# Kernel tuning notes

Measured on AMD Instinct MI355X. Metric: run time of the kernel, lower is better.

The kernel has to match this reference:

```python
import math
import jax, jax.numpy as jnp
import numpy as np

N = 50000          # nodes
E = 1_600_000      # edges
DNE = 128
DED = 128
NUM_RBF = 50
R_CUT = 5.0
LN_EPS = 1e-5


def setup_inputs() -> dict:
    key = jax.random.key(0)
    ks = jax.random.split(key, 16)
    z = jax.random.normal(ks[0], (N, 25), jnp.float32)
    edge = jax.random.randint(ks[1], (E, 2), 0, N, dtype=jnp.int64)
    r = jax.random.uniform(ks[2], (E,), jnp.float32) * (R_CUT * 1.1)  # some beyond cutoff
    u_raw = jax.random.normal(ks[3], (E, 3), jnp.float32)
    u = u_raw / jnp.linalg.norm(u_raw, axis=-1, keepdims=True)

    def xavier(k, shape):
        fan_in, fan_out = shape
        lim = math.sqrt(6.0 / (fan_in + fan_out))
        return jax.random.uniform(k, shape, jnp.float32, -lim, lim)

    return {
        "z": z, "edge": edge, "r": r, "u": u,
        "A_na_w": xavier(ks[4], (25, DNE)), "A_na_b": jnp.zeros((DNE,), jnp.float32),
        "A_nbr_w": xavier(ks[5], (25, DNE)), "A_nbr_b": jnp.zeros((DNE,), jnp.float32),
        "W_ndp_w": xavier(ks[6], (NUM_RBF, DNE)), "W_ndp_b": jnp.zeros((DNE,), jnp.float32),
        "W_nrd_w": xavier(ks[7], (2 * DNE, DNE)), "W_nrd_b": jnp.zeros((DNE,), jnp.float32),
        "W_nru_w": xavier(ks[8], (DNE, DNE)), "W_nru_b": jnp.zeros((DNE,), jnp.float32),
        "W_erp_w": xavier(ks[9], (NUM_RBF, DED)), "W_erp_b": jnp.zeros((DED,), jnp.float32),
        "ln_g": jnp.ones((DNE,), jnp.float32), "ln_b": jnp.zeros((DNE,), jnp.float32),
    }


def _sh_l2(u):
    x, y, zc = u[:, 0], u[:, 1], u[:, 2]
    s3 = math.sqrt(3.0)
    return jnp.stack([
        s3 * x * y,
        s3 * y * zc,
        0.5 * (3.0 * zc * zc - 1.0),
        s3 * zc * x,
        0.5 * s3 * (x * x - y * y),
    ], axis=-1)  # [E, 5]


def _rbf(r):
    start = math.exp(-R_CUT)
    means = jnp.linspace(start, 1.0, NUM_RBF)
    beta = (2.0 / NUM_RBF * (1.0 - start)) ** (-2)
    alpha = 5.0 / R_CUT
    return jnp.exp(-beta * (jnp.exp(-alpha * r[:, None]) - means) ** 2)  # [E, NUM_RBF]


def reference(z, edge, r, u,
              A_na_w, A_na_b, A_nbr_w, A_nbr_b,
              W_ndp_w, W_ndp_b, W_nrd_w, W_nrd_b,
              W_nru_w, W_nru_b, W_erp_w, W_erp_b,
              ln_g, ln_b):
    i, j = edge[:, 0], edge[:, 1]
    n_nodes = z.shape[0]

    # edge tensor representations (Lmax=2)
    rt0 = r[:, None]          # [E,1]
    rt1 = u                   # [E,3]
    rt2 = _sh_l2(u)           # [E,5]

    rbf = _rbf(r)                                              # [E,R]
    c = (0.5 * (jnp.cos(math.pi * r / R_CUT) + 1.0)
         * (r < R_CUT).astype(r.dtype))[:, None]               # [E,1]

    nbr = jax.nn.silu(z @ A_nbr_w + A_nbr_b)                   # [N,dne]
    gate = (rbf @ W_ndp_w + W_ndp_b) * c                       # [E,dne]
    msg = nbr[j] * gate                                        # gather + gate
    m = jax.ops.segment_sum(msg, i, num_segments=n_nodes)      # scatter-add [N,dne]

    na = jax.nn.silu(z @ A_na_w + A_na_b)
    h = jnp.concatenate([na, m], axis=-1) @ W_nrd_w + W_nrd_b  # [N,dne]
    mu = jnp.mean(h, axis=-1, keepdims=True)
    var = jnp.var(h, axis=-1, keepdims=True)
    h = (h - mu) / jnp.sqrt(var + LN_EPS) * ln_g + ln_b
    h = jax.nn.silu(h)
    h = h @ W_nru_w + W_nru_b                                  # [N,dne]

    t = (h[i] + h[j]) * (rbf @ W_erp_w + W_erp_b)              # [E,ded]
    return (h, t, rt0, rt1, rt2, c)
```

## Files before the change

### kernel.cpp

```cpp
#include <hip/hip_runtime.h>
#include <hip/hip_bf16.h>
#include <math.h>

#define NN 50000
#define NE 1600000
#define D 128
#define NRBF 50
#define RCUT 5.0f
#define LNEPS 1e-5f
#define SCAN_B 196
#define NB 16
#define NPW 8
#define EO_GRID 2048

typedef __attribute__((ext_vector_type(8))) short bf16x8;
typedef __attribute__((ext_vector_type(4))) float f32x4;

__device__ __forceinline__ float silu_f(float x) {
    return x / (1.0f + __expf(-x));
}
__device__ __forceinline__ unsigned short f2bf(float x) {
    __hip_bfloat16 b = __float2bfloat16(x);
    return *reinterpret_cast<unsigned short*>(&b);
}
__device__ __forceinline__ float bf2f(unsigned short u) {
    unsigned int x = ((unsigned int)u) << 16;
    return __uint_as_float(x);
}

__global__ __launch_bounds__(128) void nbr_kernel(
    const float* __restrict__ z, const float* __restrict__ Aw,
    const float* __restrict__ Ab, unsigned short* __restrict__ nbr_bf)
{
    const int n = blockIdx.x;
    const int d = threadIdx.x;
    float acc = Ab[d];
#pragma unroll
    for (int k = 0; k < 25; ++k)
        acc = fmaf(z[n * 25 + k], Aw[k * D + d], acc);
    nbr_bf[(size_t)n * D + d] = f2bf(silu_f(acc));
}

__global__ __launch_bounds__(256) void aux_kernel(
    const int* __restrict__ edge, const float* __restrict__ r,
    const float* __restrict__ u, float* __restrict__ rt0,
    float* __restrict__ rt1, float* __restrict__ rt2,
    float* __restrict__ cout, int* __restrict__ cnt)
{
    const int e = blockIdx.x * 256 + threadIdx.x;
    if (e >= NE) return;
    const float rr = r[e];
    __builtin_nontemporal_store(rr, &rt0[e]);
    const float cc = (rr < RCUT)
        ? 0.5f * (__cosf(3.14159265358979f * rr * (1.0f / RCUT)) + 1.0f)
        : 0.0f;
    __builtin_nontemporal_store(cc, &cout[e]);
    const float x  = u[e * 3 + 0];
    const float y  = u[e * 3 + 1];
    const float zc = u[e * 3 + 2];
    __builtin_nontemporal_store(x,  &rt1[(size_t)e * 3 + 0]);
    __builtin_nontemporal_store(y,  &rt1[(size_t)e * 3 + 1]);
    __builtin_nontemporal_store(zc, &rt1[(size_t)e * 3 + 2]);
    const float s3 = 1.7320508075688772f;
    __builtin_nontemporal_store(s3 * x * y,                  &rt2[(size_t)e * 5 + 0]);
    __builtin_nontemporal_store(s3 * y * zc,                 &rt2[(size_t)e * 5 + 1]);
    __builtin_nontemporal_store(0.5f * (3.0f * zc * zc - 1.0f), &rt2[(size_t)e * 5 + 2]);
    __builtin_nontemporal_store(s3 * zc * x,                 &rt2[(size_t)e * 5 + 3]);
    __builtin_nontemporal_store(0.5f * s3 * (x * x - y * y), &rt2[(size_t)e * 5 + 4]);
    atomicAdd(&cnt[edge[2 * e]], 1);
}

__global__ __launch_bounds__(256) void scan1_kernel(
    const int* __restrict__ cnt, int* __restrict__ off, int* __restrict__ bsum)
{
    __shared__ int s[2][256];
    const int t = threadIdx.x;
    const int g = blockIdx.x * 256 + t;
    const int v = (g < NN) ? cnt[g] : 0;
    int incl = v;
    s[0][t] = incl;
    __syncthreads();
    int cur = 0;
#pragma unroll
    for (int dd = 1; dd < 256; dd <<= 1) {
        const int add = (t >= dd) ? s[cur][t - dd] : 0;
        incl += add;
        s[cur ^ 1][t] = incl;
        __syncthreads();
        cur ^= 1;
    }
    if (g < NN) off[g] = incl - v;
    if (t == 255) bsum[blockIdx.x] = incl;
}

__global__ __launch_bounds__(256) void scan2_kernel(int* __restrict__ bsum)
{
    __shared__ int s[2][256];
    const int t = threadIdx.x;
    const int v = (t < SCAN_B) ? bsum[t] : 0;
    int incl = v;
    s[0][t] = incl;
    __syncthreads();
    int cur = 0;
#pragma unroll
    for (int dd = 1; dd < 256; dd <<= 1) {
        const int add = (t >= dd) ? s[cur][t - dd] : 0;
        incl += add;
        s[cur ^ 1][t] = incl;
        __syncthreads();
        cur ^= 1;
    }
    if (t < SCAN_B) bsum[t] = incl - v;
}

__global__ __launch_bounds__(256) void scan3_kernel(
    int* __restrict__ off, const int* __restrict__ bsum)
{
    const int g = blockIdx.x * 256 + threadIdx.x;
    if (g < NN) off[g] += bsum[blockIdx.x];
    if (g == 0) off[NN] = NE;
}

__global__ __launch_bounds__(256) void scatter_kernel(
    const int* __restrict__ edge, const float* __restrict__ r,
    const int* __restrict__ off, int* __restrict__ cursor,
    uint2* __restrict__ jr)
{
    const int e = blockIdx.x * 256 + threadIdx.x;
    if (e >= NE) return;
    const int2 ep = ((const int2*)edge)[e];
    const int pos = atomicAdd(&cursor[ep.x], 1);
    uint2 v;
    v.x = (unsigned int)ep.y;
    v.y = __float_as_uint(r[e]);
    jr[off[ep.x] + pos] = v;
}

__global__ __launch_bounds__(256, 3) void gather_msg_wave(
    const uint2* __restrict__ jr, const int* __restrict__ off,
    const float* __restrict__ W_ndp, const float* __restrict__ b_ndp,
    const unsigned short* __restrict__ nbr_bf, float* __restrict__ m)
{
    const int tid = threadIdx.x;
    const int w   = tid >> 6;
    const int l   = tid & 63;
    const int lr  = l & 15;
    const int lg  = l >> 4;

    bf16x8 wf[8][2];
#pragma unroll
    for (int dt = 0; dt < 8; ++dt) {
        const int col = lr * 8 + dt;
#pragma unroll
        for (int s = 0; s < 2; ++s) {
            bf16x8 v;
#pragma unroll
            for (int j = 0; j < 8; ++j) {
                const int k = s * 32 + lg * 8 + j;
                float wv = 0.0f;
                if (k < NRBF)       wv = W_ndp[k * D + col];
                else if (k == NRBF) wv = b_ndp[col];
                v[j] = (short)f2bf(wv);
            }
            wf[dt][s] = v;
        }
    }

    const float start = expf(-RCUT);
    const float step  = (1.0f - start) / (NRBF - 1);
    const float bq    = (2.0f / NRBF) * (1.0f - start);
    const float beta  = 1.0f / (bq * bq);

    const int wid = blockIdx.x * 4 + w;

    for (int nn = 0; nn < NPW; ++nn) {
        const int n = wid * NPW + nn;
        if (n >= NN) break;
        const int s0  = off[n];
        const int deg = off[n + 1] - s0;

        f32x4 macc[8] = {{0,0,0,0},{0,0,0,0},{0,0,0,0},{0,0,0,0},
                         {0,0,0,0},{0,0,0,0},{0,0,0,0},{0,0,0,0}};

        uint2 v = make_uint2(0u, 0u);
        if (l < 16 && l < deg) v = jr[s0 + l];

        for (int base = 0; base < deg; base += 16) {
            const bool val = (l < 16) && (base + l < deg);
            const unsigned int jv = val ? v.x : 0u;
            float er = 0.0f, cc = 0.0f;
            if (val) {
                const float rr = __uint_as_float(v.y);
                er = __expf(-rr);
                cc = (rr < RCUT)
                    ? 0.5f * (__cosf(3.14159265358979f * rr * (1.0f / RCUT)) + 1.0f)
                    : 0.0f;
            }
            uint2 vn = make_uint2(0u, 0u);
            if (l < 16 && base + 16 + l < deg) vn = jr[s0 + base + 16 + l];

            const float erL = __shfl(er, lr);
            const float ccL = __shfl(cc, lr);

            bf16x8 nv0, nv1, nv2, nv3;
            {
                const int j0 = __shfl((int)jv, lg * 4 + 0);
                const int j1 = __shfl((int)jv, lg * 4 + 1);
                const int j2 = __shfl((int)jv, lg * 4 + 2);
                const int j3 = __shfl((int)jv, lg * 4 + 3);
                nv0 = *(const bf16x8*)(nbr_bf + (size_t)j0 * D + lr * 8);
                nv1 = *(const bf16x8*)(nbr_bf + (size_t)j1 * D + lr * 8);
                nv2 = *(const bf16x8*)(nbr_bf + (size_t)j2 * D + lr * 8);
                nv3 = *(const bf16x8*)(nbr_bf + (size_t)j3 * D + lr * 8);
            }

            bf16x8 af[2];
#pragma unroll
            for (int s = 0; s < 2; ++s) {
                bf16x8 a;
#pragma unroll
                for (int j = 0; j < 8; ++j) {
                    const int k = s * 32 + lg * 8 + j;
                    float pv = 0.0f;
                    if (k < NRBF) {
                        const float diff = erL - (start + (float)k * step);
                        pv = ccL * __expf(-beta * diff * diff);
                    } else if (k == NRBF) {
                        pv = ccL;
                    }
                    a[j] = (short)f2bf(pv);
                }
                af[s] = a;
            }

#pragma unroll
            for (int dt = 0; dt < 8; ++dt) {
                f32x4 acc = {0.0f, 0.0f, 0.0f, 0.0f};
                acc = __builtin_amdgcn_mfma_f32_16x16x32_bf16(af[0], wf[dt][0], acc, 0, 0, 0);
                acc = __builtin_amdgcn_mfma_f32_16x16x32_bf16(af[1], wf[dt][1], acc, 0, 0, 0);
                macc[dt][0] = fmaf(bf2f((unsigned short)nv0[dt]), acc[0], macc[dt][0]);
                macc[dt][1] = fmaf(bf2f((unsigned short)nv1[dt]), acc[1], macc[dt][1]);
                macc[dt][2] = fmaf(bf2f((unsigned short)nv2[dt]), acc[2], macc[dt][2]);
                macc[dt][3] = fmaf(bf2f((unsigned short)nv3[dt]), acc[3], macc[dt][3]);
            }
            v = vn;
        }

        float vv[8];
#pragma unroll
        for (int dt = 0; dt < 8; ++dt) {
            float x = macc[dt][0] + macc[dt][1] + macc[dt][2] + macc[dt][3];
            x += __shfl_xor(x, 16);
            x += __shfl_xor(x, 32);
            vv[dt] = x;
        }
        if (lg == 0) {
            f32x4 o0 = {vv[0], vv[1], vv[2], vv[3]};
            f32x4 o1 = {vv[4], vv[5], vv[6], vv[7]};
            float* mp = &m[(size_t)n * D + lr * 8];
            *(f32x4*)mp       = o0;
            *(f32x4*)(mp + 4) = o1;
        }
    }
}

__global__ __launch_bounds__(256) void node_kernel2(
    const float* __restrict__ z, const float* __restrict__ A_na_w,
    const float* __restrict__ A_na_b, const float* __restrict__ m,
    const float* __restrict__ W_nrd_w, const float* __restrict__ W_nrd_b,
    const float* __restrict__ W_nru_w, const float* __restrict__ W_nru_b,
    const float* __restrict__ ln_g, const float* __restrict__ ln_b,
    float* __restrict__ hout, unsigned short* __restrict__ h_bf)
{
    __shared__ float inbuf[NB][260];
    __shared__ float wbuf[32][128];
    __shared__ float part[4][NB][2];

    const int tid = threadIdx.x;
    const int n0 = blockIdx.x * NB;
    const int nl = tid & 15;
    const int dg = tid >> 4;

    for (int idx = tid; idx < NB * 128; idx += 256) {
        const int n = idx >> 7;
        const int d = idx & 127;
        float acc = A_na_b[d];
#pragma unroll
        for (int k = 0; k < 25; ++k)
            acc = fmaf(z[(size_t)(n0 + n) * 25 + k], A_na_w[k * D + d], acc);
        inbuf[n][d]       = silu_f(acc);
        inbuf[n][128 + d] = m[(size_t)(n0 + n) * D + d];
    }

    float h1[8];
#pragma unroll
    for (int dd = 0; dd < 8; ++dd) h1[dd] = W_nrd_b[dg * 8 + dd];

    for (int tile = 0; tile < 8; ++tile) {
        __syncthreads();
        for (int v = tid; v < 32 * 32; v += 256) {
            const int row = v >> 5;
            const int c4  = (v & 31) * 4;
            *(float4*)&wbuf[row][c4] =
                *(const float4*)&W_nrd_w[(size_t)(tile * 32 + row) * D + c4];
        }
        __syncthreads();
#pragma unroll 4
        for (int k = 0; k < 32; ++k) {
            const float rin = inbuf[nl][tile * 32 + k];
            const float4 wa = *(const float4*)&wbuf[k][dg * 8];
            const float4 wb = *(const float4*)&wbuf[k][dg * 8 + 4];
            h1[0] = fmaf(rin, wa.x, h1[0]);
            h1[1] = fmaf(rin, wa.y, h1[1]);
            h1[2] = fmaf(rin, wa.z, h1[2]);
            h1[3] = fmaf(rin, wa.w, h1[3]);
            h1[4] = fmaf(rin, wb.x, h1[4]);
            h1[5] = fmaf(rin, wb.y, h1[5]);
            h1[6] = fmaf(rin, wb.z, h1[6]);
            h1[7] = fmaf(rin, wb.w, h1[7]);
        }
    }

    float s = 0.0f, sq = 0.0f;
#pragma unroll
    for (int dd = 0; dd < 8; ++dd) { s += h1[dd]; sq += h1[dd] * h1[dd]; }
    s  += __shfl_xor(s, 16);  sq += __shfl_xor(sq, 16);
    s  += __shfl_xor(s, 32);  sq += __shfl_xor(sq, 32);
    const int wv = tid >> 6;
    if ((tid & 63) < 16) { part[wv][nl][0] = s; part[wv][nl][1] = sq; }
    __syncthreads();
    float ts = 0.0f, tsq = 0.0f;
#pragma unroll
    for (int w = 0; w < 4; ++w) { ts += part[w][nl][0]; tsq += part[w][nl][1]; }
    const float mu  = ts * (1.0f / 128.0f);
    const float var = tsq * (1.0f / 128.0f) - mu * mu;
    const float inv = rsqrtf(var + LNEPS);

#pragma unroll
    for (int dd = 0; dd < 8; ++dd) {
        const int d = dg * 8 + dd;
        inbuf[nl][d] = silu_f((h1[dd] - mu) * inv * ln_g[d] + ln_b[d]);
    }

    float h2[8];
#pragma unroll
    for (int dd = 0; dd < 8; ++dd) h2[dd] = W_nru_b[dg * 8 + dd];

    for (int tile = 0; tile < 4; ++tile) {
        __syncthreads();
        for (int v = tid; v < 32 * 32; v += 256) {
            const int row = v >> 5;
            const int c4  = (v & 31) * 4;
            *(float4*)&wbuf[row][c4] =
                *(const float4*)&W_nru_w[(size_t)(tile * 32 + row) * D + c4];
        }
        __syncthreads();
#pragma unroll 4
        for (int k = 0; k < 32; ++k) {
            const float rin = inbuf[nl][tile * 32 + k];
            const float4 wa = *(const float4*)&wbuf[k][dg * 8];
            const float4 wb = *(const float4*)&wbuf[k][dg * 8 + 4];
            h2[0] = fmaf(rin, wa.x, h2[0]);
            h2[1] = fmaf(rin, wa.y, h2[1]);
            h2[2] = fmaf(rin, wa.z, h2[2]);
            h2[3] = fmaf(rin, wa.w, h2[3]);
            h2[4] = fmaf(rin, wb.x, h2[4]);
            h2[5] = fmaf(rin, wb.y, h2[5]);
            h2[6] = fmaf(rin, wb.z, h2[6]);
            h2[7] = fmaf(rin, wb.w, h2[7]);
        }
    }

    f32x4 o0 = {h2[0], h2[1], h2[2], h2[3]};
    f32x4 o1 = {h2[4], h2[5], h2[6], h2[7]};
    float* hp = &hout[(size_t)(n0 + nl) * D + dg * 8];
    __builtin_nontemporal_store(o0, (f32x4*)hp);
    __builtin_nontemporal_store(o1, (f32x4*)(hp + 4));

    unsigned int b0 = (unsigned int)f2bf(h2[0]) | ((unsigned int)f2bf(h2[1]) << 16);
    unsigned int b1 = (unsigned int)f2bf(h2[2]) | ((unsigned int)f2bf(h2[3]) << 16);
    unsigned int b2 = (unsigned int)f2bf(h2[4]) | ((unsigned int)f2bf(h2[5]) << 16);
    unsigned int b3 = (unsigned int)f2bf(h2[6]) | ((unsigned int)f2bf(h2[7]) << 16);
    *(uint4*)&h_bf[(size_t)(n0 + nl) * D + dg * 8] = make_uint4(b0, b1, b2, b3);
}

__global__ __launch_bounds__(256, 3) void edge_out_wave(
    const int* __restrict__ edge, const float* __restrict__ r,
    const float* __restrict__ W_erp, const float* __restrict__ b_erp,
    const unsigned short* __restrict__ h_bf, float* __restrict__ t)
{
    const int tid = threadIdx.x;
    const int w   = tid >> 6;
    const int l   = tid & 63;
    const int lr  = l & 15;
    const int lg  = l >> 4;

    bf16x8 wf[8][2];
    float bias[8];
#pragma unroll
    for (int dt = 0; dt < 8; ++dt) {
        const int col = lr * 8 + dt;
        bias[dt] = b_erp[col];
#pragma unroll
        for (int s = 0; s < 2; ++s) {
            bf16x8 v;
#pragma unroll
            for (int j = 0; j < 8; ++j) {
                const int k = s * 32 + lg * 8 + j;
                v[j] = (k < NRBF) ? (short)f2bf(W_erp[k * D + col]) : (short)0;
            }
            wf[dt][s] = v;
        }
    }

    const float start = expf(-RCUT);
    const float step  = (1.0f - start) / (NRBF - 1);
    const float bq    = (2.0f / NRBF) * (1.0f - start);
    const float beta  = 1.0f / (bq * bq);

    const int wid = blockIdx.x * 4 + w;
    const int nw  = gridDim.x * 4;
    const int ngroup = NE / 16;

    int2 ep = make_int2(0, 0);
    float rv = 0.0f;
    if (wid < ngroup && l < 16) {
        ep = ((const int2*)edge)[wid * 16 + l];
        rv = r[wid * 16 + l];
    }

    for (int g = wid; g < ngroup; g += nw) {
        const int iv = ep.x;
        const int jv = ep.y;
        const float er = __expf(-rv);

        int2 epn = make_int2(0, 0);
        float rvn = 0.0f;
        if (g + nw < ngroup && l < 16) {
            epn = ((const int2*)edge)[(g + nw) * 16 + l];
            rvn = r[(g + nw) * 16 + l];
        }

        const float erL = __shfl(er, lr);

        bf16x8 hi0, hi1, hi2, hi3, hj0, hj1, hj2, hj3;
        {
            const int i0 = __shfl(iv, lg * 4 + 0), j0 = __shfl(jv, lg * 4 + 0);
            const int i1 = __shfl(iv, lg * 4 + 1), j1 = __shfl(jv, lg * 4 + 1);
            const int i2 = __shfl(iv, lg * 4 + 2), j2 = __shfl(jv, lg * 4 + 2);
            const int i3 = __shfl(iv, lg * 4 + 3), j3 = __shfl(jv, lg * 4 + 3);
            hi0 = *(const bf16x8*)(h_bf + (size_t)i0 * D + lr * 8);
            hj0 = *(const bf16x8*)(h_bf + (size_t)j0 * D + lr * 8);
            hi1 = *(const bf16x8*)(h_bf + (size_t)i1 * D + lr * 8);
            hj1 = *(const bf16x8*)(h_bf + (size_t)j1 * D + lr * 8);
            hi2 = *(const bf16x8*)(h_bf + (size_t)i2 * D + lr * 8);
            hj2 = *(const bf16x8*)(h_bf + (size_t)j2 * D + lr * 8);
            hi3 = *(const bf16x8*)(h_bf + (size_t)i3 * D + lr * 8);
            hj3 = *(const bf16x8*)(h_bf + (size_t)j3 * D + lr * 8);
        }

        bf16x8 af[2];
#pragma unroll
        for (int s = 0; s < 2; ++s) {
            bf16x8 a;
#pragma unroll
            for (int j = 0; j < 8; ++j) {
                const int k = s * 32 + lg * 8 + j;
                float pv = 0.0f;
                if (k < NRBF) {
                    const float diff = erL - (start + (float)k * step);
                    pv = __expf(-beta * diff * diff);
                }
                a[j] = (short)f2bf(pv);
            }
            af[s] = a;
        }

        f32x4 accs[8];
#pragma unroll
        for (int dt = 0; dt < 8; ++dt) {
            f32x4 acc = {0.0f, 0.0f, 0.0f, 0.0f};
            acc = __builtin_amdgcn_mfma_f32_16x16x32_bf16(af[0], wf[dt][0], acc, 0, 0, 0);
            acc = __builtin_amdgcn_mfma_f32_16x16x32_bf16(af[1], wf[dt][1], acc, 0, 0, 0);
            accs[dt] = acc;
        }

        const int eb = g * 16;
#pragma unroll
        for (int q = 0; q < 4; ++q) {
            const bf16x8 hi8 = (q == 0) ? hi0 : (q == 1) ? hi1 : (q == 2) ? hi2 : hi3;
            const bf16x8 hj8 = (q == 0) ? hj0 : (q == 1) ? hj1 : (q == 2) ? hj2 : hj3;
            float o[8];
#pragma unroll
            for (int dt = 0; dt < 8; ++dt) {
                const float hvf = bf2f((unsigned short)hi8[dt]) + bf2f((unsigned short)hj8[dt]);
                o[dt] = hvf * (accs[dt][q] + bias[dt]);
            }
            f32x4 o0 = {o[0], o[1], o[2], o[3]};
            f32x4 o1 = {o[4], o[5], o[6], o[7]};
            float* tp = &t[(size_t)(eb + lg * 4 + q) * D + lr * 8];
            __builtin_nontemporal_store(o0, (f32x4*)tp);
            __builtin_nontemporal_store(o1, (f32x4*)(tp + 4));
        }

        ep = epn;
        rv = rvn;
    }
}

extern "C" void kernel_launch(void* const* d_in, const int* in_sizes, int n_in,
                              void* d_out, int out_size, void* d_ws, size_t ws_size,
                              hipStream_t stream) {
    const float* z      = (const float*)d_in[0];
    const int*   edge   = (const int*)d_in[1];
    const float* r      = (const float*)d_in[2];
    const float* u      = (const float*)d_in[3];
    const float* A_na_w  = (const float*)d_in[4];
    const float* A_na_b  = (const float*)d_in[5];
    const float* A_nbr_w = (const float*)d_in[6];
    const float* A_nbr_b = (const float*)d_in[7];
    const float* W_ndp_w = (const float*)d_in[8];
    const float* W_ndp_b = (const float*)d_in[9];
    const float* W_nrd_w = (const float*)d_in[10];
    const float* W_nrd_b = (const float*)d_in[11];
    const float* W_nru_w = (const float*)d_in[12];
    const float* W_nru_b = (const float*)d_in[13];
    const float* W_erp_w = (const float*)d_in[14];
    const float* W_erp_b = (const float*)d_in[15];
    const float* ln_g    = (const float*)d_in[16];
    const float* ln_b    = (const float*)d_in[17];

    float* out = (float*)d_out;
    float* h_out   = out;
    float* t_out   = out + (size_t)NN * D;
    float* rt0_out = t_out + (size_t)NE * D;
    float* rt1_out = rt0_out + (size_t)NE;
    float* rt2_out = rt1_out + (size_t)NE * 3;
    float* c_out   = rt2_out + (size_t)NE * 5;

    unsigned short* nbr_bf = (unsigned short*)d_ws;
    float* m_ws   = (float*)((char*)d_ws + (size_t)NN * D * sizeof(unsigned short));
    unsigned short* h_bf = (unsigned short*)((char*)m_ws + (size_t)NN * D * sizeof(float));

    uint2* jr   = (uint2*)t_out;
    int* off    = (int*)(jr + NE);
    int* cursor = off + (NN + 1);
    int* bsum   = cursor + NN;

    hipMemsetAsync(cursor, 0, (size_t)NN * sizeof(int), stream);

    nbr_kernel<<<NN, 128, 0, stream>>>(z, A_nbr_w, A_nbr_b, nbr_bf);

    aux_kernel<<<(NE + 255) / 256, 256, 0, stream>>>(
        edge, r, u, rt0_out, rt1_out, rt2_out, c_out, cursor);

    scan1_kernel<<<SCAN_B, 256, 0, stream>>>(cursor, off, bsum);
    scan2_kernel<<<1, 256, 0, stream>>>(bsum);
    scan3_kernel<<<SCAN_B, 256, 0, stream>>>(off, bsum);

    hipMemsetAsync(cursor, 0, (size_t)NN * sizeof(int), stream);

    scatter_kernel<<<(NE + 255) / 256, 256, 0, stream>>>(edge, r, off, cursor, jr);

    {
        const int nwaves = (NN + NPW - 1) / NPW;
        const int blocks = (nwaves + 3) / 4;
        gather_msg_wave<<<blocks, 256, 0, stream>>>(
            jr, off, W_ndp_w, W_ndp_b, nbr_bf, m_ws);
    }

    node_kernel2<<<NN / NB, 256, 0, stream>>>(
        z, A_na_w, A_na_b, m_ws, W_nrd_w, W_nrd_b,
        W_nru_w, W_nru_b, ln_g, ln_b, h_out, h_bf);

    edge_out_wave<<<EO_GRID, 256, 0, stream>>>(
        edge, r, W_erp_w, W_erp_b, h_bf, t_out);
}
```

Before: 840.5 us.

## Split gather and edge-output kernels into four column passes

Both the message-gather and edge-output kernels now handle 32 of the 128 feature columns per launch, and each runs four times. The intent is to shrink the working set of gathered node rows per pass so it fits in cache, and to cut register pressure enough to allow occupancy 4 instead of 3. In exchange, edge indices, r, RBF expansions and the MFMA A-operands are recomputed four times, and every gathered row costs four 4-byte loads instead of one 16-byte vector load. The t stores also become narrow 8-byte strided writes.

Result: no change. 850.9 us (+1.2%).

```diff
diff --git a/kernel.cpp b/kernel.cpp
--- a/kernel.cpp
+++ b/kernel.cpp
@@ -12,9 +12,11 @@
 #define NB 16
 #define NPW 8
 #define EO_GRID 2048
+#define NPASS 4
 
 typedef __attribute__((ext_vector_type(8))) short bf16x8;
 typedef __attribute__((ext_vector_type(4))) float f32x4;
+typedef __attribute__((ext_vector_type(2))) float f32x2;
 
 __device__ __forceinline__ float silu_f(float x) {
     return x / (1.0f + __expf(-x));
@@ -136,21 +138,23 @@
     jr[off[ep.x] + pos] = v;
 }
 
-__global__ __launch_bounds__(256, 3) void gather_msg_wave(
+__global__ __launch_bounds__(256, 4) void gather_msg_wave(
     const uint2* __restrict__ jr, const int* __restrict__ off,
     const float* __restrict__ W_ndp, const float* __restrict__ b_ndp,
-    const unsigned short* __restrict__ nbr_bf, float* __restrict__ m)
+    const unsigned short* __restrict__ nbr_bf, float* __restrict__ m,
+    const int pass)
 {
     const int tid = threadIdx.x;
     const int w   = tid >> 6;
     const int l   = tid & 63;
     const int lr  = l & 15;
     const int lg  = l >> 4;
-
-    bf16x8 wf[8][2];
-#pragma unroll
-    for (int dt = 0; dt < 8; ++dt) {
-        const int col = lr * 8 + dt;
+    const int c0  = pass * 32 + lr * 2;
+
+    bf16x8 wf[2][2];
+#pragma unroll
+    for (int dt = 0; dt < 2; ++dt) {
+        const int col = c0 + dt;
 #pragma unroll
         for (int s = 0; s < 2; ++s) {
             bf16x8 v;
@@ -179,8 +183,8 @@
         const int s0  = off[n];
         const int deg = off[n + 1] - s0;
 
-        f32x4 macc[8] = {{0,0,0,0},{0,0,0,0},{0,0,0,0},{0,0,0,0},
-                         {0,0,0,0},{0,0,0,0},{0,0,0,0},{0,0,0,0}};
+        f32x4 macc0 = {0, 0, 0, 0};
+        f32x4 macc1 = {0, 0, 0, 0};
 
         uint2 v = make_uint2(0u, 0u);
         if (l < 16 && l < deg) v = jr[s0 + l];
@@ -202,16 +206,16 @@
             const float erL = __shfl(er, lr);
             const float ccL = __shfl(cc, lr);
 
-            bf16x8 nv0, nv1, nv2, nv3;
+            unsigned int nv0, nv1, nv2, nv3;
             {
                 const int j0 = __shfl((int)jv, lg * 4 + 0);
                 const int j1 = __shfl((int)jv, lg * 4 + 1);
                 const int j2 = __shfl((int)jv, lg * 4 + 2);
                 const int j3 = __shfl((int)jv, lg * 4 + 3);
-                nv0 = *(const bf16x8*)(nbr_bf + (size_t)j0 * D + lr * 8);
-                nv1 = *(const bf16x8*)(nbr_bf + (size_t)j1 * D + lr * 8);
-                nv2 = *(const bf16x8*)(nbr_bf + (size_t)j2 * D + lr * 8);
-                nv3 = *(const bf16x8*)(nbr_bf + (size_t)j3 * D + lr * 8);
+                nv0 = *(const unsigned int*)(nbr_bf + (size_t)j0 * D + c0);
+                nv1 = *(const unsigned int*)(nbr_bf + (size_t)j1 * D + c0);
+                nv2 = *(const unsigned int*)(nbr_bf + (size_t)j2 * D + c0);
+                nv3 = *(const unsigned int*)(nbr_bf + (size_t)j3 * D + c0);
             }
 
             bf16x8 af[2];
@@ -233,33 +237,32 @@
                 af[s] = a;
             }
 
-#pragma unroll
-            for (int dt = 0; dt < 8; ++dt) {
-                f32x4 acc = {0.0f, 0.0f, 0.0f, 0.0f};
-                acc = __builtin_amdgcn_mfma_f32_16x16x32_bf16(af[0], wf[dt][0], acc, 0, 0, 0);
-                acc = __builtin_amdgcn_mfma_f32_16x16x32_bf16(af[1], wf[dt][1], acc, 0, 0, 0);
-                macc[dt][0] = fmaf(bf2f((unsigned short)nv0[dt]), acc[0], macc[dt][0]);
-                macc[dt][1] = fmaf(bf2f((unsigned short)nv1[dt]), acc[1], macc[dt][1]);
-                macc[dt][2] = fmaf(bf2f((unsigned short)nv2[dt]), acc[2], macc[dt][2]);
-                macc[dt][3] = fmaf(bf2f((unsigned short)nv3[dt]), acc[3], macc[dt][3]);
-            }
+            f32x4 acc0 = {0, 0, 0, 0};
+            acc0 = __builtin_amdgcn_mfma_f32_16x16x32_bf16(af[0], wf[0][0], acc0, 0, 0, 0);
+            acc0 = __builtin_amdgcn_mfma_f32_16x16x32_bf16(af[1], wf[0][1], acc0, 0, 0, 0);
+            f32x4 acc1 = {0, 0, 0, 0};
+            acc1 = __builtin_amdgcn_mfma_f32_16x16x32_bf16(af[0], wf[1][0], acc1, 0, 0, 0);
+            acc1 = __builtin_amdgcn_mfma_f32_16x16x32_bf16(af[1], wf[1][1], acc1, 0, 0, 0);
+
+            macc0[0] = fmaf(bf2f((unsigned short)(nv0 & 0xffff)), acc0[0], macc0[0]);
+            macc1[0] = fmaf(bf2f((unsigned short)(nv0 >> 16)),    acc1[0], macc1[0]);
+            macc0[1] = fmaf(bf2f((unsigned short)(nv1 & 0xffff)), acc0[1], macc0[1]);
+            macc1[1] = fmaf(bf2f((unsigned short)(nv1 >> 16)),    acc1[1], macc1[1]);
+            macc0[2] = fmaf(bf2f((unsigned short)(nv2 & 0xffff)), acc0[2], macc0[2]);
+            macc1[2] = fmaf(bf2f((unsigned short)(nv2 >> 16)),    acc1[2], macc1[2]);
+            macc0[3] = fmaf(bf2f((unsigned short)(nv3 & 0xffff)), acc0[3], macc0[3]);
+            macc1[3] = fmaf(bf2f((unsigned short)(nv3 >> 16)),    acc1[3], macc1[3]);
+
             v = vn;
         }
 
-        float vv[8];
-#pragma unroll
-        for (int dt = 0; dt < 8; ++dt) {
-            float x = macc[dt][0] + macc[dt][1] + macc[dt][2] + macc[dt][3];
-            x += __shfl_xor(x, 16);
-            x += __shfl_xor(x, 32);
-            vv[dt] = x;
-        }
+        float v0 = macc0[0] + macc0[1] + macc0[2] + macc0[3];
+        float v1 = macc1[0] + macc1[1] + macc1[2] + macc1[3];
+        v0 += __shfl_xor(v0, 16); v0 += __shfl_xor(v0, 32);
+        v1 += __shfl_xor(v1, 16); v1 += __shfl_xor(v1, 32);
         if (lg == 0) {
-            f32x4 o0 = {vv[0], vv[1], vv[2], vv[3]};
-            f32x4 o1 = {vv[4], vv[5], vv[6], vv[7]};
-            float* mp = &m[(size_t)n * D + lr * 8];
-            *(f32x4*)mp       = o0;
-            *(f32x4*)(mp + 4) = o1;
+            f32x2 o = {v0, v1};
+            *(f32x2*)&m[(size_t)n * D + c0] = o;
         }
     }
 }
@@ -384,22 +387,24 @@
     *(uint4*)&h_bf[(size_t)(n0 + nl) * D + dg * 8] = make_uint4(b0, b1, b2, b3);
 }
 
-__global__ __launch_bounds__(256, 3) void edge_out_wave(
+__global__ __launch_bounds__(256, 4) void edge_out_wave(
     const int* __restrict__ edge, const float* __restrict__ r,
     const float* __restrict__ W_erp, const float* __restrict__ b_erp,
-    const unsigned short* __restrict__ h_bf, float* __restrict__ t)
+    const unsigned short* __restrict__ h_bf, float* __restrict__ t,
+    const int pass)
 {
     const int tid = threadIdx.x;
     const int w   = tid >> 6;
     const int l   = tid & 63;
     const int lr  = l & 15;
     const int lg  = l >> 4;
-
-    bf16x8 wf[8][2];
-    float bias[8];
-#pragma unroll
-    for (int dt = 0; dt < 8; ++dt) {
-        const int col = lr * 8 + dt;
+    const int c0  = pass * 32 + lr * 2;
+
+    bf16x8 wf[2][2];
+    float bias[2];
+#pragma unroll
+    for (int dt = 0; dt < 2; ++dt) {
+        const int col = c0 + dt;
         bias[dt] = b_erp[col];
 #pragma unroll
         for (int s = 0; s < 2; ++s) {
@@ -443,20 +448,20 @@
 
         const float erL = __shfl(er, lr);
 
-        bf16x8 hi0, hi1, hi2, hi3, hj0, hj1, hj2, hj3;
+        unsigned int hi0, hi1, hi2, hi3, hj0, hj1, hj2, hj3;
         {
             const int i0 = __shfl(iv, lg * 4 + 0), j0 = __shfl(jv, lg * 4 + 0);
             const int i1 = __shfl(iv, lg * 4 + 1), j1 = __shfl(jv, lg * 4 + 1);
             const int i2 = __shfl(iv, lg * 4 + 2), j2 = __shfl(jv, lg * 4 + 2);
             const int i3 = __shfl(iv, lg * 4 + 3), j3 = __shfl(jv, lg * 4 + 3);
-            hi0 = *(const bf16x8*)(h_bf + (size_t)i0 * D + lr * 8);
-            hj0 = *(const bf16x8*)(h_bf + (size_t)j0 * D + lr * 8);
-            hi1 = *(const bf16x8*)(h_bf + (size_t)i1 * D + lr * 8);
-            hj1 = *(const bf16x8*)(h_bf + (size_t)j1 * D + lr * 8);
-            hi2 = *(const bf16x8*)(h_bf + (size_t)i2 * D + lr * 8);
-            hj2 = *(const bf16x8*)(h_bf + (size_t)j2 * D + lr * 8);
-            hi3 = *(const bf16x8*)(h_bf + (size_t)i3 * D + lr * 8);
-            hj3 = *(const bf16x8*)(h_bf + (size_t)j3 * D + lr * 8);
+            hi0 = *(const unsigned int*)(h_bf + (size_t)i0 * D + c0);
+            hj0 = *(const unsigned int*)(h_bf + (size_t)j0 * D + c0);
+            hi1 = *(const unsigned int*)(h_bf + (size_t)i1 * D + c0);
+            hj1 = *(const unsigned int*)(h_bf + (size_t)j1 * D + c0);
+            hi2 = *(const unsigned int*)(h_bf + (size_t)i2 * D + c0);
+            hj2 = *(const unsigned int*)(h_bf + (size_t)j2 * D + c0);
+            hi3 = *(const unsigned int*)(h_bf + (size_t)i3 * D + c0);
+            hj3 = *(const unsigned int*)(h_bf + (size_t)j3 * D + c0);
         }
 
         bf16x8 af[2];
@@ -476,31 +481,25 @@
             af[s] = a;
         }
 
-        f32x4 accs[8];
-#pragma unroll
-        for (int dt = 0; dt < 8; ++dt) {
-            f32x4 acc = {0.0f, 0.0f, 0.0f, 0.0f};
-            acc = __builtin_amdgcn_mfma_f32_16x16x32_bf16(af[0], wf[dt][0], acc, 0, 0, 0);
-            acc = __builtin_amdgcn_mfma_f32_16x16x32_bf16(af[1], wf[dt][1], acc, 0, 0, 0);
-            accs[dt] = acc;
-        }
+        f32x4 acc0 = {0, 0, 0, 0};
+        acc0 = __builtin_amdgcn_mfma_f32_16x16x32_bf16(af[0], wf[0][0], acc0, 0, 0, 0);
+        acc0 = __builtin_amdgcn_mfma_f32_16x16x32_bf16(af[1], wf[0][1], acc0, 0, 0, 0);
+        f32x4 acc1 = {0, 0, 0, 0};
+        acc1 = __builtin_amdgcn_mfma_f32_16x16x32_bf16(af[0], wf[1][0], acc1, 0, 0, 0);
+        acc1 = __builtin_amdgcn_mfma_f32_16x16x32_bf16(af[1], wf[1][1], acc1, 0, 0, 0);
 
         const int eb = g * 16;
 #pragma unroll
         for (int q = 0; q < 4; ++q) {
-            const bf16x8 hi8 = (q == 0) ? hi0 : (q == 1) ? hi1 : (q == 2) ? hi2 : hi3;
-            const bf16x8 hj8 = (q == 0) ? hj0 : (q == 1) ? hj1 : (q == 2) ? hj2 : hj3;
-            float o[8];
-#pragma unroll
-            for (int dt = 0; dt < 8; ++dt) {
-                const float hvf = bf2f((unsigned short)hi8[dt]) + bf2f((unsigned short)hj8[dt]);
-                o[dt] = hvf * (accs[dt][q] + bias[dt]);
-            }
-            f32x4 o0 = {o[0], o[1], o[2], o[3]};
-            f32x4 o1 = {o[4], o[5], o[6], o[7]};
-            float* tp = &t[(size_t)(eb + lg * 4 + q) * D + lr * 8];
-            __builtin_nontemporal_store(o0, (f32x4*)tp);
-            __builtin_nontemporal_store(o1, (f32x4*)(tp + 4));
+            const unsigned int hiq = (q == 0) ? hi0 : (q == 1) ? hi1 : (q == 2) ? hi2 : hi3;
+            const unsigned int hjq = (q == 0) ? hj0 : (q == 1) ? hj1 : (q == 2) ? hj2 : hj3;
+            const float hv0 = bf2f((unsigned short)(hiq & 0xffff))
+                            + bf2f((unsigned short)(hjq & 0xffff));
+            const float hv1 = bf2f((unsigned short)(hiq >> 16))
+                            + bf2f((unsigned short)(hjq >> 16));
+            f32x2 o = {hv0 * (acc0[q] + bias[0]), hv1 * (acc1[q] + bias[1])};
+            float* tp = &t[(size_t)(eb + lg * 4 + q) * D + c0];
+            __builtin_nontemporal_store(o, (f32x2*)tp);
         }
 
         ep = epn;
@@ -565,14 +564,16 @@
     {
         const int nwaves = (NN + NPW - 1) / NPW;
         const int blocks = (nwaves + 3) / 4;
-        gather_msg_wave<<<blocks, 256, 0, stream>>>(
-            jr, off, W_ndp_w, W_ndp_b, nbr_bf, m_ws);
+        for (int pass = 0; pass < NPASS; ++pass)
+            gather_msg_wave<<<blocks, 256, 0, stream>>>(
+                jr, off, W_ndp_w, W_ndp_b, nbr_bf, m_ws, pass);
     }
 
     node_kernel2<<<NN / NB, 256, 0, stream>>>(
         z, A_na_w, A_na_b, m_ws, W_nrd_w, W_nrd_b,
         W_nru_w, W_nru_b, ln_g, ln_b, h_out, h_bf);
 
-    edge_out_wave<<<EO_GRID, 256, 0, stream>>>(
-        edge, r, W_erp_w, W_erp_b, h_bf, t_out);
-}
+    for (int pass = 0; pass < NPASS; ++pass)
+        edge_out_wave<<<EO_GRID, 256, 0, stream>>>(
+            edge, r, W_erp_w, W_erp_b, h_bf, t_out, pass);
+}
```
